# Performance work log

Hardware: AMD Instinct MI355X
Metric: run time of the kernel (lower is better)

Reference implementation:

```python
import jax, jax.numpy as jnp
import numpy as np
from jax.scipy.ndimage import map_coordinates

N = 512      # image H=W (x0.shape[2])
A = 30       # number of projection angles (sparse-view CT)
D = 729      # det_count (hardcoded in source)
L = 3        # LayerNo
B = 2        # batch
P = 2048     # FFT padding: next pow2 >= 2*D


def _ramp_filter(size):
    # standard Ram-Lak filter built in spatial domain (skimage/torch-radon style)
    n = np.concatenate((np.arange(1, size // 2 + 1, 2), np.arange(size // 2 - 1, 0, -2)))
    f = np.zeros(size)
    f[0] = 0.25
    f[1::2] = -1.0 / (np.pi * n) ** 2
    return jnp.asarray(2.0 * np.real(np.fft.fft(f))[: size // 2 + 1], dtype=jnp.float32)


def setup_inputs() -> dict:
    key = jax.random.key(0)
    ks = jax.random.split(key, 8)
    x0 = jax.random.normal(ks[0], (B, 1, N, N), jnp.float32)
    sinogram = jax.random.normal(ks[1], (B, 1, A, D), jnp.float32)
    theta = jnp.linspace(0.0, np.pi, A, endpoint=False).astype(jnp.float32)
    theta_label = theta
    # denoiser params, stacked over L unrolled layers
    w1 = jax.random.normal(ks[2], (L, 32, 1, 3, 3), jnp.float32) * 0.1
    b1 = jnp.zeros((L, 32), jnp.float32)
    w2 = jax.random.normal(ks[3], (L, 32, 32, 3, 3), jnp.float32) * 0.05
    b2 = jnp.zeros((L, 32), jnp.float32)
    w3 = jax.random.normal(ks[4], (L, 32, 32, 3, 3), jnp.float32) * 0.05
    b3 = jnp.zeros((L, 32), jnp.float32)
    w4 = jax.random.normal(ks[5], (L, 1, 32, 3, 3), jnp.float32) * 0.05
    steps = jnp.ones((L,), jnp.float32)  # step_n params (requires_grad=False)
    return {"cond": 1, "x0": x0, "sinogram": sinogram, "theta": theta,
            "theta_label": theta_label, "w1": w1, "b1": b1, "w2": w2, "b2": b2,
            "w3": w3, "b3": b3, "w4": w4, "steps": steps}


def _conv(x, w, b=None):
    y = jax.lax.conv_general_dilated(x, w, (1, 1), 'SAME',
                                     dimension_numbers=('NCHW', 'OIHW', 'NCHW'))
    return y if b is None else y + b[None, :, None, None]


def _denoiser(x, w1, b1, w2, b2, w3, b3, w4):
    h = jax.nn.relu(_conv(x, w1, b1))
    h = jax.nn.relu(_conv(h, w2, b2))
    h = jax.nn.relu(_conv(h, w3, b3))
    return _conv(h, w4)


def _geometry(theta):
    # parallel-beam ray sampling grid: rows/cols [A, D, T] with T=D samples (dt=1)
    c = (N - 1) / 2.0
    s = jnp.arange(D, dtype=jnp.float32) - (D - 1) / 2.0  # detector coords
    t = s                                                  # along-ray samples
    cs, sn = jnp.cos(theta), jnp.sin(theta)
    x = s[None, :, None] * cs[:, None, None] - t[None, None, :] * sn[:, None, None]
    y = s[None, :, None] * sn[:, None, None] + t[None, None, :] * cs[:, None, None]
    return y + c, x + c  # rows, cols


def _radon_fwd(imgs, rows, cols):
    # imgs [B,N,N] -> sinogram [B,A,D] via bilinear line-integral sampling
    sample = lambda im: map_coordinates(im, [rows, cols], order=1, mode='constant', cval=0.0)
    return jax.vmap(sample)(imgs).sum(-1)


def _filter_sino(sino, filt):
    F = jnp.fft.rfft(sino, n=P, axis=-1)
    g = jnp.fft.irfft(F * filt, n=P, axis=-1)[..., :D]
    return g * (jnp.pi / (2.0 * A))  # FBP normalization


def _backproj(sino, theta):
    # sino [B,A,D] -> image [B,N,N], linear interp along detector axis
    c = (N - 1) / 2.0
    xs = jnp.arange(N, dtype=jnp.float32) - c
    cs, sn = jnp.cos(theta), jnp.sin(theta)
    sgrid = cs[:, None, None] * xs[None, None, :] + sn[:, None, None] * xs[None, :, None]  # [A,N,N]
    idx = sgrid + (D - 1) / 2.0
    lo = jnp.floor(idx).astype(jnp.int32)
    w = idx - lo
    lo_ok = (lo >= 0) & (lo < D)
    hi_ok = (lo + 1 >= 0) & (lo + 1 < D)
    lo_c = jnp.clip(lo, 0, D - 1)
    hi_c = jnp.clip(lo + 1, 0, D - 1)
    a = jnp.arange(A)[:, None, None]
    v = sino[:, a, lo_c] * jnp.where(lo_ok, 1.0 - w, 0.0) + \
        sino[:, a, hi_c] * jnp.where(hi_ok, w, 0.0)       # [B,A,N,N]
    return v.sum(axis=1)


def reference(cond, x0, sinogram, theta, theta_label, w1, b1, w2, b2, w3, b3, w4, steps):
    rows, cols = _geometry(theta)
    filt = _ramp_filter(P)
    X = x0[:, 0]           # [B,N,N]
    sino = sinogram[:, 0]  # [B,A,D]
    for n in range(L):
        sino_pred = _radon_fwd(X, rows, cols)
        filtered = _filter_sino(sino_pred, filt)
        outputs = _backproj(sino - filtered, theta)
        z = X + steps[n] * outputs
        noise = _denoiser(X[:, None], w1[n], b1[n], w2[n], b2[n], w3[n], b3[n], w4[n])[:, 0]
        filtered_noise = _filter_sino(_radon_fwd(noise, rows, cols), filt)
        outputs_noise = _backproj(filtered_noise, theta)
        X = z + noise - steps[n] * outputs_noise
    Xo = X[:, None]
    return (Xo, Xo, Xo)
```

## Files before the change

### kernel.cpp

```cpp
#include <hip/hip_runtime.h>
#include <hip/hip_bf16.h>

typedef __hip_bfloat16 bf16;
typedef __attribute__((ext_vector_type(8))) short short8;
typedef __attribute__((ext_vector_type(4))) short s4v;
typedef __attribute__((ext_vector_type(4))) float float4v;

#define NN 512
#define NA 30
#define ND 729
#define NB 2
#define NL 3
#define BNN (NB*NN*NN)
#define BAD (NB*NA*ND)

#define PW 520
#define PH 516
#define PIMG (PH*PW)
#define POFF (2*PW + 2)

#define O_CS  0
#define O_SN  32
#define O_ICS 64
#define O_ISN 96
#define O_XP  128
#define O_YP  (O_XP + 2*PIMG)
#define O_YPT (O_YP + 2*PIMG)
#define O_SP  (O_YPT + 2*PIMG)
#define O_Q   (O_SP + BAD)
#define O_WR  (O_Q + BAD)
#define O_H   (((O_WR + 34560) + 15) & ~15)
#define H_FLOATS (NB * 32 * NN * NN / 2)

#define WR2_OFF 0
#define WR3_OFF 27648
#define WR4_OFF 55296

__device__ __forceinline__ float2 ld2u(const float* p)
{
    float2 r;
    __builtin_memcpy(&r, p, 8);
    return r;
}

__global__ void k_prep(const float* __restrict__ theta,
                       const float* __restrict__ w2, const float* __restrict__ w3,
                       const float* __restrict__ w4, const float* __restrict__ x0,
                       float* __restrict__ ws, bf16* __restrict__ wr)
{
    int idx = blockIdx.x * 256 + threadIdx.x;
    if (idx < NA) {
        float t = theta[idx];
        float cs = cosf(t), sn = sinf(t);
        ws[O_CS + idx] = cs;
        ws[O_SN + idx] = sn;
        ws[O_ICS + idx] = 1.0f / cs;
        ws[O_ISN + idx] = -1.0f / sn;
    }
    if (idx < 2 * 27648) {
        const float* w = (idx < 27648) ? w2 : w3;
        int base = (idx < 27648) ? WR2_OFF : WR3_OFF;
        int r = idx % 27648;
        int n = r / 9216; int r2 = r % 9216;
        int tap = r2 / 1024; int r3 = r2 % 1024;
        int co = r3 / 32, ci = r3 % 32;
        wr[base + r] = __float2bfloat16(w[n * 9216 + (co * 32 + ci) * 9 + tap]);
    } else if (idx < 2 * 27648 + 3 * 4608) {
        int r = idx - 2 * 27648;
        int n = r / 4608; int r2 = r % 4608;
        int tap = r2 / 512; int r3 = r2 % 512;
        int co = r3 / 32, ci = r3 % 32;
        float v = (co == 0) ? w4[n * 288 + ci * 9 + tap] : 0.f;
        wr[WR4_OFF + r] = __float2bfloat16(v);
    }
    if (idx < 2 * PIMG) {
        int b = idx / PIMG, p = idx % PIMG;
        int y = p / PW, x = p % PW;
        bool interior = (y >= 2 && y < 2 + NN && x >= 2 && x < 2 + NN);
        float v = interior ? x0[b * NN * NN + (y - 2) * NN + (x - 2)] : 0.f;
        ws[O_XP + idx] = v;
        if (!interior) {
            ws[O_YP + idx] = 0.f;
            ws[O_YPT + idx] = 0.f;
        }
    }
}

__device__ __forceinline__ void isect2(float A, float inv, float lo, float hi,
                                       float& tlo, float& thi)
{
    float a = (lo - A) * inv, b = (hi - A) * inv;
    tlo = fmaxf(tlo, fminf(a, b));
    thi = fminf(thi, fmaxf(a, b));
}

__global__ __launch_bounds__(256) void k_radon(const float* __restrict__ img,
    const float* __restrict__ imgT, const float* __restrict__ ws,
    float* __restrict__ out)
{
    int b = blockIdx.z, a = blockIdx.y;
    int wave = threadIdx.x >> 6;
    int lane = threadIdx.x & 63;
    int half = lane >> 5, tl = lane & 31;
    int s = blockIdx.x * 8 + wave * 2 + half;
    float cs = ws[O_CS + a], sn = ws[O_SN + a];
    float ics = ws[O_ICS + a], isn = ws[O_ISN + a];
    float s_c = (float)s - 364.0f;
    float A_r = 255.5f + s_c * sn;
    float A_c = 255.5f + s_c * cs;

    float tlo = -1e9f, thi = 1e9f;
    isect2(A_r, ics, -1.0f, 512.0f, tlo, thi);
    isect2(A_c, isn, -1.0f, 512.0f, tlo, thi);
    float t0f = fmaxf(tlo + 364.0f, 0.0f);
    float t1f = fminf(thi + 364.0f, 728.0f);

    bool useT = fabsf(cs) >= fabsf(sn);
    const float* im = (useT ? imgT : img) + b * PIMG;

    float acc = 0.f;
    if (s < ND && t0f <= t1f) {
        int tb = (int)ceilf(t0f);
        int te = (int)floorf(t1f);
#pragma unroll 2
        for (int t = tb + tl; t <= te; t += 32) {
            float tc = (float)t - 364.0f;
            float r = fmaf(tc, cs, A_r);
            float c = fmaf(-tc, sn, A_c);
            float rf = floorf(r), cf = floorf(c);
            float dr = r - rf, dc = c - cf;
            int irr = (int)rf, icc = (int)cf;
            int idx = useT ? (icc * PW + irr) : (irr * PW + icc);
            float da = useT ? dr : dc;
            float db = useT ? dc : dr;
            float2 p1 = ld2u(im + idx);
            float2 p2 = ld2u(im + idx + PW);
            float u = fmaf(da, p1.y - p1.x, p1.x);
            float w = fmaf(da, p2.y - p2.x, p2.x);
            acc = fmaf(db, w - u, acc + u);
        }
    }
    acc += __shfl_xor(acc, 16, 64);
    acc += __shfl_xor(acc, 8, 64);
    acc += __shfl_xor(acc, 4, 64);
    acc += __shfl_xor(acc, 2, 64);
    acc += __shfl_xor(acc, 1, 64);
    if (tl == 0 && s < ND) out[(b * NA + a) * ND + s] = acc;
}

__global__ void k_filter(const float* __restrict__ sp, const float* __restrict__ sino,
                         float* __restrict__ q)
{
    __shared__ float row[ND];
    __shared__ float taps[364];
    int ba = blockIdx.y;
    const float* src = sp + ba * ND;
    for (int i = threadIdx.x; i < ND; i += 256) row[i] = src[i];
    const float PI2 = 9.86960440108936f;
    for (int i = threadIdx.x; i < 364; i += 256) {
        float m = (float)(2 * i + 1);
        taps[i] = -2.0f / (PI2 * m * m);
    }
    __syncthreads();
    const float scale = 0.0523598775598299f;
    int d = blockIdx.x * 256 + threadIdx.x;
    if (d < ND) {
        float g0 = 0.5f * row[d], g1 = 0.f;
#pragma unroll 4
        for (int j = 0; j < 364; j += 2) {
            int m0 = 2 * j + 1, m1 = 2 * j + 3;
            float l0 = (d - m0 >= 0) ? row[d - m0] : 0.f;
            float r0 = (d + m0 < ND) ? row[d + m0] : 0.f;
            g0 = fmaf(taps[j], l0 + r0, g0);
            float l1 = (d - m1 >= 0) ? row[d - m1] : 0.f;
            float r1 = (d + m1 < ND) ? row[d + m1] : 0.f;
            g1 = fmaf(taps[j + 1], l1 + r1, g1);
        }
        q[ba * ND + d] = sino[ba * ND + d] - scale * (g0 + g1);
    }
}

__global__ __launch_bounds__(256) void k_backproj_update(const float* __restrict__ q,
    const float* __restrict__ src1, const float* __restrict__ ws,
    const float* __restrict__ steps, int n, float* __restrict__ out,
    float* __restrict__ outcopy)
{
    __shared__ float qt[NA][28];
    __shared__ int dmin_s[NA];
    int b = blockIdx.z;
    int x0 = blockIdx.x * 16, y0 = blockIdx.y * 16;
    int tid = threadIdx.x;
    int lx = tid & 15, ly = tid >> 4;
    const float* qb = q + b * NA * ND;

    for (int idx = tid; idx < NA * 26; idx += 256) {
        int a = idx / 26, j = idx % 26;
        float cs = ws[O_CS + a], sn = ws[O_SN + a];
        float f00 = fmaf(cs, (float)x0 - 255.5f, fmaf(sn, (float)y0 - 255.5f, 364.0f));
        float fmn = f00 + fminf(cs * 15.f, 0.f) + fminf(sn * 15.f, 0.f);
        int dm = (int)floorf(fmn);
        if (j == 0) dmin_s[a] = dm;
        int d = dm + j;
        qt[a][j] = (d >= 0 && d < ND) ? qb[a * ND + d] : 0.f;
    }
    __syncthreads();

    float xc = (float)(x0 + lx) - 255.5f, yc = (float)(y0 + ly) - 255.5f;
    float acc = 0.f;
#pragma unroll
    for (int a = 0; a < NA; a++) {
        float cs = ws[O_CS + a], sn = ws[O_SN + a];
        float f = fmaf(cs, xc, fmaf(sn, yc, 364.0f));
        float lf = floorf(f);
        float w = f - lf;
        int j = (int)lf - dmin_s[a];
        float v0 = qt[a][j], v1 = qt[a][j + 1];
        acc = fmaf(v0, 1.0f - w, fmaf(v1, w, acc));
    }
    int pidx = b * PIMG + (y0 + ly) * PW + (x0 + lx);
    float v = fmaf(steps[n], acc, src1[pidx]);
    out[pidx] = v;
    if (outcopy) {
        int fidx = b * NN * NN + (y0 + ly) * NN + (x0 + lx);
        outcopy[fidx] = v;
        outcopy[fidx + BNN] = v;
        outcopy[fidx + 2 * BNN] = v;
    }
}

__global__ __launch_bounds__(256) void k_conv12(const float* __restrict__ XPb,
    const float* __restrict__ W1, const float* __restrict__ B1,
    const bf16* __restrict__ Wr2, const float* __restrict__ B2,
    bf16* __restrict__ outb)
{
    __shared__ bf16 h1t[34][18][32];
    int b = blockIdx.z;
    int x0 = blockIdx.x * 16;
    int Y0 = blockIdx.y * 32;
    const float* in = XPb + b * PIMG;

    for (int p = threadIdx.x; p < 34 * 18; p += 256) {
        int yy = p / 18, xx = p % 18;
        int gy = Y0 + yy - 1, gx = x0 + xx - 1;
        if (gy < 0 || gy >= NN || gx < 0 || gx >= NN) {
#pragma unroll
            for (int g = 0; g < 4; g++)
                *(short8*)(&h1t[yy][xx][g * 8]) = short8{};
        } else {
            float v[9];
#pragma unroll
            for (int dy = 0; dy < 3; dy++)
#pragma unroll
                for (int dx = 0; dx < 3; dx++)
                    v[dy * 3 + dx] = in[(gy + dy - 1) * PW + (gx + dx - 1)];
#pragma unroll
            for (int g = 0; g < 4; g++) {
                short8 pk;
#pragma unroll
                for (int j = 0; j < 8; j++) {
                    int co = g * 8 + j;
                    float a = B1[co];
                    const float* w = W1 + co * 9;
#pragma unroll
                    for (int k = 0; k < 9; k++) a = fmaf(v[k], w[k], a);
                    a = fmaxf(a, 0.f);
                    bf16 h = __float2bfloat16(a);
                    pk[j] = *reinterpret_cast<short*>(&h);
                }
                *(short8*)(&h1t[yy][xx][g * 8]) = pk;
            }
        }
    }
    __syncthreads();

    int lane = threadIdx.x & 63;
    int wave = threadIdx.x >> 6;
    int n16 = lane & 15, quad = lane >> 4;
    int y0w = Y0 + wave * 8;

    short8 wf[18];
#pragma unroll
    for (int tap = 0; tap < 9; tap++)
#pragma unroll
        for (int t = 0; t < 2; t++)
            wf[tap * 2 + t] = *(const short8*)(Wr2 + ((tap * 2 + t) * 16 + n16) * 32 + quad * 8);

    short8 win[3][3];
    auto loadrow = [&](int yy, short8* dst) {
        int ly = yy - (Y0 - 1);
#pragma unroll
        for (int dx = 0; dx < 3; dx++)
            dst[dx] = *(const short8*)(&h1t[ly][n16 + dx][quad * 8]);
    };
    loadrow(y0w - 1, win[0]);
    loadrow(y0w,     win[1]);

    float4v bias[2];
#pragma unroll
    for (int t = 0; t < 2; t++)
        bias[t] = *(const float4v*)(B2 + t * 16 + quad * 4);

    bf16* out = outb + (size_t)b * NN * NN * 32;
#pragma unroll
    for (int i = 0; i < 8; i++) {
        int y = y0w + i;
        loadrow(y + 1, win[(i + 2) % 3]);
        float4v acc[2];
#pragma unroll
        for (int t = 0; t < 2; t++) acc[t] = bias[t];
#pragma unroll
        for (int dy = 0; dy < 3; dy++) {
            short8* row = win[(i + dy) % 3];
#pragma unroll
            for (int dx = 0; dx < 3; dx++) {
                int tap = dy * 3 + dx;
#pragma unroll
                for (int t = 0; t < 2; t++)
                    acc[t] = __builtin_amdgcn_mfma_f32_16x16x32_bf16(wf[tap * 2 + t], row[dx], acc[t], 0, 0, 0);
            }
        }
        bf16* pp = out + ((size_t)y * NN + x0 + n16) * 32 + quad * 4;
#pragma unroll
        for (int t = 0; t < 2; t++) {
            s4v pk;
#pragma unroll
            for (int r = 0; r < 4; r++) {
                float v = fmaxf(acc[t][r], 0.f);
                bf16 h = __float2bfloat16(v);
                pk[r] = *reinterpret_cast<short*>(&h);
            }
            *(s4v*)(pp + t * 16) = pk;
        }
    }
}

#define SH 8
template<int NCO, bool RELU, bool HASB, bool OUTF32>
__global__ __launch_bounds__(256) void k_conv_stream(const bf16* __restrict__ inb,
    const bf16* __restrict__ Wr, const float* __restrict__ Bs,
    const float* __restrict__ addsrc, void* __restrict__ outv,
    float* __restrict__ outT)
{
    int lane = threadIdx.x & 63;
    int wave = threadIdx.x >> 6;
    int n16 = lane & 15, quad = lane >> 4;
    int b = blockIdx.z;
    int x0 = blockIdx.x * 16;
    int y0 = (blockIdx.y * 4 + wave) * SH;
    const bf16* in = inb + (size_t)b * NN * NN * 32;

    short8 wf[9 * NCO];
#pragma unroll
    for (int tap = 0; tap < 9; tap++)
#pragma unroll
        for (int t = 0; t < NCO; t++)
            wf[tap * NCO + t] = *(const short8*)(Wr + ((tap * NCO + t) * 16 + n16) * 32 + quad * 8);

    bool vx[3];
#pragma unroll
    for (int dx = 0; dx < 3; dx++) {
        int xx = x0 + n16 + dx - 1;
        vx[dx] = (xx >= 0) && (xx < NN);
    }

    short8 win[3][3];
    auto loadrow = [&](int yy, short8* dst) {
        if (yy >= 0 && yy < NN) {
            const bf16* rowp = in + (size_t)yy * NN * 32;
#pragma unroll
            for (int dx = 0; dx < 3; dx++) {
                short8 v = {};
                if (vx[dx]) v = *(const short8*)(rowp + (x0 + n16 + dx - 1) * 32 + quad * 8);
                dst[dx] = v;
            }
        } else {
            dst[0] = short8{}; dst[1] = short8{}; dst[2] = short8{};
        }
    };
    loadrow(y0 - 1, win[0]);
    loadrow(y0,     win[1]);

    float4v bias[NCO];
#pragma unroll
    for (int t = 0; t < NCO; t++)
        bias[t] = HASB ? *(const float4v*)(Bs + t * 16 + quad * 4) : (float4v){0.f, 0.f, 0.f, 0.f};

#pragma unroll
    for (int i = 0; i < SH; i++) {
        int y = y0 + i;
        loadrow(y + 1, win[(i + 2) % 3]);
        float4v acc[NCO];
#pragma unroll
        for (int t = 0; t < NCO; t++) acc[t] = bias[t];
#pragma unroll
        for (int dy = 0; dy < 3; dy++) {
            short8* row = win[(i + dy) % 3];
#pragma unroll
            for (int dx = 0; dx < 3; dx++) {
                int tap = dy * 3 + dx;
#pragma unroll
                for (int t = 0; t < NCO; t++)
                    acc[t] = __builtin_amdgcn_mfma_f32_16x16x32_bf16(wf[tap * NCO + t], row[dx], acc[t], 0, 0, 0);
            }
        }
        if (OUTF32) {
            float* out = (float*)outv + b * PIMG;
            if (quad == 0) {
                int px = x0 + n16;
                float vv = addsrc[b * PIMG + y * PW + px] + acc[0][0];
                out[y * PW + px] = vv;
                outT[b * PIMG + px * PW + y] = vv;
            }
        } else {
            bf16* out = (bf16*)outv + (size_t)b * NN * NN * 32;
            bf16* pp = out + ((size_t)y * NN + x0 + n16) * 32 + quad * 4;
#pragma unroll
            for (int t = 0; t < NCO; t++) {
                s4v pk;
#pragma unroll
                for (int r = 0; r < 4; r++) {
                    float v = acc[t][r];
                    if (RELU) v = fmaxf(v, 0.f);
                    bf16 h = __float2bfloat16(v);
                    pk[r] = *reinterpret_cast<short*>(&h);
                }
                *(s4v*)(pp + t * 16) = pk;
            }
        }
    }
}

extern "C" void kernel_launch(void* const* d_in, const int* in_sizes, int n_in,
                              void* d_out, int out_size, void* d_ws, size_t ws_size,
                              hipStream_t stream)
{
    const float* x0    = (const float*)d_in[1];
    const float* sg    = (const float*)d_in[2];
    const float* theta = (const float*)d_in[3];
    const float* w1    = (const float*)d_in[5];
    const float* b1    = (const float*)d_in[6];
    const float* w2    = (const float*)d_in[7];
    const float* b2    = (const float*)d_in[8];
    const float* w3    = (const float*)d_in[9];
    const float* b3    = (const float*)d_in[10];
    const float* w4    = (const float*)d_in[11];
    const float* steps = (const float*)d_in[12];

    float* ws = (float*)d_ws;
    float* XP  = ws + O_XP + POFF;
    float* YP  = ws + O_YP + POFF;
    float* YPT = ws + O_YPT + POFF;
    float* SP = ws + O_SP;
    float* Q  = ws + O_Q;
    bf16* wr  = (bf16*)(ws + O_WR);
    bf16* h1  = (bf16*)(ws + O_H);
    bf16* h2  = (bf16*)(ws + O_H + H_FLOATS);

    k_prep<<<(2 * PIMG + 255) / 256, 256, 0, stream>>>(theta, w2, w3, w4, x0, ws, wr);

    for (int n = 0; n < NL; n++) {
        k_conv12<<<dim3(32, 16, NB), 256, 0, stream>>>(
            XP, w1 + n * 288, b1 + n * 32, wr + WR2_OFF + n * 9216, b2 + n * 32, h2);
        k_conv_stream<2, true, true, false><<<dim3(32, 16, NB), 256, 0, stream>>>(
            h2, wr + WR3_OFF + n * 9216, b3 + n * 32, nullptr, h1, nullptr);
        k_conv_stream<1, false, false, true><<<dim3(32, 16, NB), 256, 0, stream>>>(
            h1, wr + WR4_OFF + n * 4608, nullptr, XP, YP, YPT);

        k_radon<<<dim3((ND + 7) / 8, NA, NB), 256, 0, stream>>>(YP, YPT, ws, SP);
        k_filter<<<dim3(3, NB * NA), 256, 0, stream>>>(SP, sg, Q);
        k_backproj_update<<<dim3(32, 32, NB), 256, 0, stream>>>(
            Q, YP, ws, steps, n, XP, (n == NL - 1) ? (float*)d_out : nullptr);
    }
}
```

Measured before the change: 415.4 us.

## Fuse denoiser conv3 and conv4 into one kernel with LDS row ring

Replaces the separate conv3 and conv4 kernel launches with one kernel that computes conv3 rows (with halo) into a 3-row shared-memory ring buffer in bf16. It then immediately applies conv4 from LDS and writes the residual-added output plus its transpose. This removes the global write and re-read of the 32-channel h1 intermediate and one launch per layer. In exchange it recomputes halo columns and rows, uses a smaller grid (512 blocks) with two syncs per row, and has uneven per-wave work on the halo group.

New measurement: 443.1 us. +6.7%, slower.

```diff
diff --git a/kernel.cpp b/kernel.cpp
--- a/kernel.cpp
+++ b/kernel.cpp
@@ -334,6 +334,122 @@
     }
 }
 
+#define C34_W 128
+#define C34_H 8
+#define C34_PX 130
+#define H3S 40
+
+__global__ __launch_bounds__(256) void k_conv34(const bf16* __restrict__ inb,
+    const bf16* __restrict__ Wr3, const float* __restrict__ B3,
+    const bf16* __restrict__ Wr4, const float* __restrict__ addsrc,
+    float* __restrict__ outY, float* __restrict__ outT)
+{
+    __shared__ bf16 h3s[3][C34_PX][H3S];
+    int lane = threadIdx.x & 63;
+    int wave = threadIdx.x >> 6;
+    int n16 = lane & 15, quad = lane >> 4;
+    int b = blockIdx.z;
+    int x0 = blockIdx.x * C34_W;
+    int y0 = blockIdx.y * C34_H;
+    const bf16* in = inb + (size_t)b * NN * NN * 32;
+
+    short8 wf3[18];
+#pragma unroll
+    for (int tap = 0; tap < 9; tap++)
+#pragma unroll
+        for (int t = 0; t < 2; t++)
+            wf3[tap * 2 + t] = *(const short8*)(Wr3 + ((tap * 2 + t) * 16 + n16) * 32 + quad * 8);
+    short8 wf4[9];
+#pragma unroll
+    for (int tap = 0; tap < 9; tap++)
+        wf4[tap] = *(const short8*)(Wr4 + (tap * 16 + n16) * 32 + quad * 8);
+
+    float4v bias3[2];
+#pragma unroll
+    for (int t = 0; t < 2; t++)
+        bias3[t] = *(const float4v*)(B3 + t * 16 + quad * 4);
+
+    for (int r = 0; r < C34_H + 2; r++) {
+        int slot = r % 3;
+        int hy = y0 - 1 + r;
+        bool rowv = (hy >= 0) && (hy < NN);
+        int gcnt = 2 + (((r & 3) == wave) ? 1 : 0);
+        for (int k = 0; k < gcnt; k++) {
+            int g = (k < 2) ? (wave + k * 4) : 8;
+            int pxi = g * 16 + n16;
+            int gxb = x0 + pxi - 2;
+            short8 wband[3][3];
+#pragma unroll
+            for (int dy = 0; dy < 3; dy++) {
+                int gy = hy - 1 + dy;
+                bool yv = (gy >= 0) && (gy < NN);
+                const bf16* rowp = in + (size_t)gy * NN * 32;
+#pragma unroll
+                for (int dx = 0; dx < 3; dx++) {
+                    int gx = gxb + dx;
+                    short8 v = {};
+                    if (yv && gx >= 0 && gx < NN)
+                        v = *(const short8*)(rowp + gx * 32 + quad * 8);
+                    wband[dy][dx] = v;
+                }
+            }
+            float4v a3[2] = {bias3[0], bias3[1]};
+#pragma unroll
+            for (int dy = 0; dy < 3; dy++)
+#pragma unroll
+                for (int dx = 0; dx < 3; dx++) {
+                    int tap = dy * 3 + dx;
+#pragma unroll
+                    for (int t = 0; t < 2; t++)
+                        a3[t] = __builtin_amdgcn_mfma_f32_16x16x32_bf16(wf3[tap * 2 + t], wband[dy][dx], a3[t], 0, 0, 0);
+                }
+            int gcol = x0 + pxi - 1;
+            bool cv = rowv && (gcol >= 0) && (gcol < NN);
+            if (pxi < C34_PX) {
+#pragma unroll
+                for (int t = 0; t < 2; t++) {
+                    s4v pk = {};
+                    if (cv) {
+#pragma unroll
+                        for (int r2 = 0; r2 < 4; r2++) {
+                            float v = fmaxf(a3[t][r2], 0.f);
+                            bf16 h = __float2bfloat16(v);
+                            pk[r2] = *reinterpret_cast<short*>(&h);
+                        }
+                    }
+                    *(s4v*)(&h3s[slot][pxi][t * 16 + quad * 4]) = pk;
+                }
+            }
+        }
+        __syncthreads();
+        if (r >= 2) {
+            int y = y0 + r - 2;
+#pragma unroll
+            for (int k = 0; k < 2; k++) {
+                int g4 = wave * 2 + k;
+                float4v a4 = {0.f, 0.f, 0.f, 0.f};
+#pragma unroll
+                for (int dy = 0; dy < 3; dy++) {
+                    int sl = (r - 2 + dy) % 3;
+#pragma unroll
+                    for (int dx = 0; dx < 3; dx++) {
+                        short8 hv = *(const short8*)(&h3s[sl][g4 * 16 + n16 + dx][quad * 8]);
+                        a4 = __builtin_amdgcn_mfma_f32_16x16x32_bf16(wf4[dy * 3 + dx], hv, a4, 0, 0, 0);
+                    }
+                }
+                if (quad == 0) {
+                    int px = x0 + g4 * 16 + n16;
+                    int pidx = b * PIMG + y * PW + px;
+                    float vv = addsrc[pidx] + a4[0];
+                    outY[pidx] = vv;
+                    outT[b * PIMG + px * PW + y] = vv;
+                }
+            }
+        }
+        __syncthreads();
+    }
+}
+
 #define SH 8
 template<int NCO, bool RELU, bool HASB, bool OUTF32>
 __global__ __launch_bounds__(256) void k_conv_stream(const bf16* __restrict__ inb,
@@ -453,7 +569,6 @@
     float* SP = ws + O_SP;
     float* Q  = ws + O_Q;
     bf16* wr  = (bf16*)(ws + O_WR);
-    bf16* h1  = (bf16*)(ws + O_H);
     bf16* h2  = (bf16*)(ws + O_H + H_FLOATS);
 
     k_prep<<<(2 * PIMG + 255) / 256, 256, 0, stream>>>(theta, w2, w3, w4, x0, ws, wr);
@@ -461,10 +576,9 @@
     for (int n = 0; n < NL; n++) {
         k_conv12<<<dim3(32, 16, NB), 256, 0, stream>>>(
             XP, w1 + n * 288, b1 + n * 32, wr + WR2_OFF + n * 9216, b2 + n * 32, h2);
-        k_conv_stream<2, true, true, false><<<dim3(32, 16, NB), 256, 0, stream>>>(
-            h2, wr + WR3_OFF + n * 9216, b3 + n * 32, nullptr, h1, nullptr);
-        k_conv_stream<1, false, false, true><<<dim3(32, 16, NB), 256, 0, stream>>>(
-            h1, wr + WR4_OFF + n * 4608, nullptr, XP, YP, YPT);
+        k_conv34<<<dim3(4, 64, NB), 256, 0, stream>>>(
+            h2, wr + WR3_OFF + n * 9216, b3 + n * 32, wr + WR4_OFF + n * 4608,
+            XP, YP, YPT);
 
         k_radon<<<dim3((ND + 7) / 8, NA, NB), 256, 0, stream>>>(YP, YPT, ws, SP);
         k_filter<<<dim3(3, NB * NA), 256, 0, stream>>>(SP, sg, Q);
```

## Fuse conv3 and conv4 into one kernel with halo tile kept in LDS

Applied to the files above, without the earlier changes.

Replaces the two separate streaming conv kernels for the third and fourth denoiser layers with one fused kernel. Each block computes a 64x8 output tile: five waves produce conv3 activations for a 66x10 haloed region into shared memory, then four waves apply conv4 from LDS and write the residual update. This removes the round trip of the 32-channel bf16 intermediate through global memory and one launch per layer, at the cost of recomputing halo rows and columns, idle waves in phase two, and an LDS footprint that limits occupancy.

Result: no change. 413.5 us (-0.5%).

```diff
diff --git a/kernel.cpp b/kernel.cpp
--- a/kernel.cpp
+++ b/kernel.cpp
@@ -334,97 +334,135 @@
     }
 }
 
-#define SH 8
-template<int NCO, bool RELU, bool HASB, bool OUTF32>
-__global__ __launch_bounds__(256) void k_conv_stream(const bf16* __restrict__ inb,
-    const bf16* __restrict__ Wr, const float* __restrict__ Bs,
-    const float* __restrict__ addsrc, void* __restrict__ outv,
-    float* __restrict__ outT)
-{
+#define C34_W 64
+#define C34_H 8
+#define C34_PX 66
+#define H3S 40
+
+__global__ __launch_bounds__(320, 3) void k_conv34(const bf16* __restrict__ inb,
+    const bf16* __restrict__ Wr3, const float* __restrict__ B3,
+    const bf16* __restrict__ Wr4, const float* __restrict__ addsrc,
+    float* __restrict__ outY, float* __restrict__ outT)
+{
+    __shared__ bf16 h3s[10][C34_PX][H3S];
     int lane = threadIdx.x & 63;
     int wave = threadIdx.x >> 6;
     int n16 = lane & 15, quad = lane >> 4;
     int b = blockIdx.z;
-    int x0 = blockIdx.x * 16;
-    int y0 = (blockIdx.y * 4 + wave) * SH;
+    int x0 = blockIdx.x * C34_W;
+    int y0 = blockIdx.y * C34_H;
     const bf16* in = inb + (size_t)b * NN * NN * 32;
 
-    short8 wf[9 * NCO];
-#pragma unroll
-    for (int tap = 0; tap < 9; tap++)
-#pragma unroll
-        for (int t = 0; t < NCO; t++)
-            wf[tap * NCO + t] = *(const short8*)(Wr + ((tap * NCO + t) * 16 + n16) * 32 + quad * 8);
-
-    bool vx[3];
-#pragma unroll
-    for (int dx = 0; dx < 3; dx++) {
-        int xx = x0 + n16 + dx - 1;
-        vx[dx] = (xx >= 0) && (xx < NN);
-    }
-
-    short8 win[3][3];
-    auto loadrow = [&](int yy, short8* dst) {
-        if (yy >= 0 && yy < NN) {
-            const bf16* rowp = in + (size_t)yy * NN * 32;
-#pragma unroll
-            for (int dx = 0; dx < 3; dx++) {
-                short8 v = {};
-                if (vx[dx]) v = *(const short8*)(rowp + (x0 + n16 + dx - 1) * 32 + quad * 8);
-                dst[dx] = v;
-            }
-        } else {
-            dst[0] = short8{}; dst[1] = short8{}; dst[2] = short8{};
-        }
-    };
-    loadrow(y0 - 1, win[0]);
-    loadrow(y0,     win[1]);
-
-    float4v bias[NCO];
-#pragma unroll
-    for (int t = 0; t < NCO; t++)
-        bias[t] = HASB ? *(const float4v*)(Bs + t * 16 + quad * 4) : (float4v){0.f, 0.f, 0.f, 0.f};
-
-#pragma unroll
-    for (int i = 0; i < SH; i++) {
-        int y = y0 + i;
-        loadrow(y + 1, win[(i + 2) % 3]);
-        float4v acc[NCO];
-#pragma unroll
-        for (int t = 0; t < NCO; t++) acc[t] = bias[t];
-#pragma unroll
-        for (int dy = 0; dy < 3; dy++) {
-            short8* row = win[(i + dy) % 3];
-#pragma unroll
-            for (int dx = 0; dx < 3; dx++) {
-                int tap = dy * 3 + dx;
-#pragma unroll
-                for (int t = 0; t < NCO; t++)
-                    acc[t] = __builtin_amdgcn_mfma_f32_16x16x32_bf16(wf[tap * NCO + t], row[dx], acc[t], 0, 0, 0);
-            }
-        }
-        if (OUTF32) {
-            float* out = (float*)outv + b * PIMG;
+    {
+        short8 wf3[18];
+#pragma unroll
+        for (int tap = 0; tap < 9; tap++)
+#pragma unroll
+            for (int t = 0; t < 2; t++)
+                wf3[tap * 2 + t] = *(const short8*)(Wr3 + ((tap * 2 + t) * 16 + n16) * 32 + quad * 8);
+        float4v bias3[2];
+#pragma unroll
+        for (int t = 0; t < 2; t++)
+            bias3[t] = *(const float4v*)(B3 + t * 16 + quad * 4);
+
+        int pxi = wave * 16 + n16;
+        int gx0 = x0 + pxi - 2;
+        bool cvx[3];
+#pragma unroll
+        for (int dx = 0; dx < 3; dx++) {
+            int gx = gx0 + dx;
+            cvx[dx] = (gx >= 0) && (gx < NN);
+        }
+        bool pxok = pxi < C34_PX;
+        int gcol = x0 + pxi - 1;
+        bool colv = pxok && (gcol >= 0) && (gcol < NN);
+
+        short8 win[3][3];
+        auto ldrow = [&](int gy, short8* dst) {
+            if (gy >= 0 && gy < NN) {
+                const bf16* rowp = in + (size_t)gy * NN * 32 + quad * 8;
+#pragma unroll
+                for (int dx = 0; dx < 3; dx++) {
+                    short8 v = {};
+                    if (cvx[dx]) v = *(const short8*)(rowp + (size_t)(gx0 + dx) * 32);
+                    dst[dx] = v;
+                }
+            } else {
+                dst[0] = short8{}; dst[1] = short8{}; dst[2] = short8{};
+            }
+        };
+        ldrow(y0 - 2, win[0]);
+        ldrow(y0 - 1, win[1]);
+#pragma unroll
+        for (int r = 0; r < 10; r++) {
+            int hy = y0 - 1 + r;
+            ldrow(hy + 1, win[(r + 2) % 3]);
+            float4v a3[2] = {bias3[0], bias3[1]};
+#pragma unroll
+            for (int dy = 0; dy < 3; dy++) {
+                short8* row = win[(r + dy) % 3];
+#pragma unroll
+                for (int dx = 0; dx < 3; dx++) {
+                    int tap = dy * 3 + dx;
+#pragma unroll
+                    for (int t = 0; t < 2; t++)
+                        a3[t] = __builtin_amdgcn_mfma_f32_16x16x32_bf16(wf3[tap * 2 + t], row[dx], a3[t], 0, 0, 0);
+                }
+            }
+            bool rowv = (hy >= 0) && (hy < NN);
+            bool live = rowv && colv;
+            if (pxok) {
+#pragma unroll
+                for (int t = 0; t < 2; t++) {
+                    s4v pk = {};
+                    if (live) {
+#pragma unroll
+                        for (int r2 = 0; r2 < 4; r2++) {
+                            float v = fmaxf(a3[t][r2], 0.f);
+                            bf16 h = __float2bfloat16(v);
+                            pk[r2] = *reinterpret_cast<short*>(&h);
+                        }
+                    }
+                    *(s4v*)(&h3s[r][pxi][t * 16 + quad * 4]) = pk;
+                }
+            }
+        }
+    }
+    __syncthreads();
+
+    if (wave < 4) {
+        short8 wf4[9];
+#pragma unroll
+        for (int tap = 0; tap < 9; tap++)
+            wf4[tap] = *(const short8*)(Wr4 + (tap * 16 + n16) * 32 + quad * 8);
+
+        int c = wave * 16 + n16;
+        short8 hw[3][3];
+        auto ldh = [&](int r, short8* dst) {
+#pragma unroll
+            for (int dx = 0; dx < 3; dx++)
+                dst[dx] = *(const short8*)(&h3s[r][c + dx][quad * 8]);
+        };
+        ldh(0, hw[0]);
+        ldh(1, hw[1]);
+#pragma unroll
+        for (int i = 0; i < 8; i++) {
+            ldh(i + 2, hw[(i + 2) % 3]);
+            float4v a4 = {0.f, 0.f, 0.f, 0.f};
+#pragma unroll
+            for (int dy = 0; dy < 3; dy++) {
+                short8* row = hw[(i + dy) % 3];
+#pragma unroll
+                for (int dx = 0; dx < 3; dx++)
+                    a4 = __builtin_amdgcn_mfma_f32_16x16x32_bf16(wf4[dy * 3 + dx], row[dx], a4, 0, 0, 0);
+            }
             if (quad == 0) {
-                int px = x0 + n16;
-                float vv = addsrc[b * PIMG + y * PW + px] + acc[0][0];
-                out[y * PW + px] = vv;
+                int px = x0 + c;
+                int y = y0 + i;
+                int pidx = b * PIMG + y * PW + px;
+                float vv = addsrc[pidx] + a4[0];
+                outY[pidx] = vv;
                 outT[b * PIMG + px * PW + y] = vv;
-            }
-        } else {
-            bf16* out = (bf16*)outv + (size_t)b * NN * NN * 32;
-            bf16* pp = out + ((size_t)y * NN + x0 + n16) * 32 + quad * 4;
-#pragma unroll
-            for (int t = 0; t < NCO; t++) {
-                s4v pk;
-#pragma unroll
-                for (int r = 0; r < 4; r++) {
-                    float v = acc[t][r];
-                    if (RELU) v = fmaxf(v, 0.f);
-                    bf16 h = __float2bfloat16(v);
-                    pk[r] = *reinterpret_cast<short*>(&h);
-                }
-                *(s4v*)(pp + t * 16) = pk;
             }
         }
     }
@@ -453,7 +491,6 @@
     float* SP = ws + O_SP;
     float* Q  = ws + O_Q;
     bf16* wr  = (bf16*)(ws + O_WR);
-    bf16* h1  = (bf16*)(ws + O_H);
     bf16* h2  = (bf16*)(ws + O_H + H_FLOATS);
 
     k_prep<<<(2 * PIMG + 255) / 256, 256, 0, stream>>>(theta, w2, w3, w4, x0, ws, wr);
@@ -461,10 +498,9 @@
     for (int n = 0; n < NL; n++) {
         k_conv12<<<dim3(32, 16, NB), 256, 0, stream>>>(
             XP, w1 + n * 288, b1 + n * 32, wr + WR2_OFF + n * 9216, b2 + n * 32, h2);
-        k_conv_stream<2, true, true, false><<<dim3(32, 16, NB), 256, 0, stream>>>(
-            h2, wr + WR3_OFF + n * 9216, b3 + n * 32, nullptr, h1, nullptr);
-        k_conv_stream<1, false, false, true><<<dim3(32, 16, NB), 256, 0, stream>>>(
-            h1, wr + WR4_OFF + n * 4608, nullptr, XP, YP, YPT);
+        k_conv34<<<dim3(8, 64, NB), 320, 0, stream>>>(
+            h2, wr + WR3_OFF + n * 9216, b3 + n * 32, wr + WR4_OFF + n * 4608,
+            XP, YP, YPT);
 
         k_radon<<<dim3((ND + 7) / 8, NA, NB), 256, 0, stream>>>(YP, YPT, ws, SP);
         k_filter<<<dim3(3, NB * NA), 256, 0, stream>>>(SP, sg, Q);
```
